# Optimization experiments

Measured on AMD Instinct MI355X. Metric: run time of the kernel, lower is better.

The kernel has to match this reference:

```python
import jax, jax.numpy as jnp
import numpy as np

NUM_HEADS = 12

def setup_inputs() -> dict:
    key = jax.random.key(0)
    ks = jax.random.split(key, 5)
    B, S, E = 1, 4096, 768
    x = jax.random.normal(ks[0], (B, S, E), dtype=jnp.float32)
    Wqkv = jax.random.normal(ks[1], (3 * E, E), dtype=jnp.float32) * (E ** -0.5)
    bqkv = jax.random.normal(ks[2], (3 * E,), dtype=jnp.float32) * 0.02
    Wo = jax.random.normal(ks[3], (E, E), dtype=jnp.float32) * (E ** -0.5)
    bo = jax.random.normal(ks[4], (E,), dtype=jnp.float32) * 0.02
    return {"x": x, "Wqkv": Wqkv, "bqkv": bqkv, "Wo": Wo, "bo": bo, "window_size": 128}

def reference(x, Wqkv, bqkv, Wo, bo, window_size):
    B, S, E = x.shape
    H = NUM_HEADS
    hd = E // H
    # qkv projection: [B,S,3E] -> [B,S,H,3*hd] -> split
    qkv = (x @ Wqkv.T + bqkv).reshape(B, S, H, 3 * hd)
    q, k, v = jnp.split(qkv, 3, axis=-1)  # each [B,S,H,hd]
    q = q.transpose(0, 2, 1, 3)  # [B,H,S,hd]
    k = k.transpose(0, 2, 1, 3)
    v = v.transpose(0, 2, 1, 3)
    # dense scores, masked to local window |i-j| <= window_size
    scores = jnp.einsum('bhqd,bhkd->bhqk', q, k) / (hd ** 0.5)
    idx = jnp.arange(S)
    in_window = jnp.abs(idx[:, None] - idx[None, :]) <= window_size  # [S,S]
    scores = jnp.where(in_window[None, None, :, :], scores, -jnp.inf)
    attn = jax.nn.softmax(scores, axis=-1)
    out = jnp.einsum('bhqk,bhkd->bhqd', attn, v)  # [B,H,S,hd]
    out = out.transpose(0, 2, 1, 3).reshape(B, S, E)
    return out @ Wo.T + bo
```

## Files before the change

kernel.cpp:

```cpp
#include <hip/hip_runtime.h>


typedef __attribute__((ext_vector_type(8))) short short8;
typedef __attribute__((ext_vector_type(4))) short short4v;
typedef __attribute__((ext_vector_type(4))) float f32x4;

#define S_LEN 4096
#define EMB   768
#define NH    12
#define HD    64
#define QT    64
#define WMAX  128
#define NKT   20
#define QSCALE 0.18033688f

#if defined(__HIP_DEVICE_COMPILE__)
#define MFMA16(a, b, c) __builtin_amdgcn_mfma_f32_16x16x16bf16_1k(a, b, c, 0, 0, 0)
#else
#define MFMA16(a, b, c) (c)
#endif

__device__ __forceinline__ short f2bf(float f) {
    union { unsigned int i; float f; } c;
    c.f = f;
    unsigned int i = c.i;
    unsigned int r = (i + 0x7FFFu + ((i >> 16) & 1u)) >> 16;
    return (short)(unsigned short)r;
}

#define NX4  (S_LEN * EMB / 4)
#define NW4  (3 * EMB * EMB / 4)
#define NO4  (EMB * EMB / 4)
__global__ __launch_bounds__(256) void convert_all(
    const float* __restrict__ x, const float* __restrict__ wqkv,
    const float* __restrict__ wo, short* __restrict__ xb,
    short* __restrict__ wqkvb, short* __restrict__ wob)
{
    int i = blockIdx.x * 256 + threadIdx.x;
    const float* src; short* dst; int off;
    if (i < NX4)            { src = x;    dst = xb;    off = i; }
    else if (i < NX4 + NW4) { src = wqkv; dst = wqkvb; off = i - NX4; }
    else                    { src = wo;   dst = wob;   off = i - NX4 - NW4; }
    float4 v = ((const float4*)src)[off];
    short4v o = { f2bf(v.x), f2bf(v.y), f2bf(v.z), f2bf(v.w) };
    *(short4v*)(dst + (size_t)off * 4) = o;
}

__global__ __launch_bounds__(256) void gemm_qkv(
    const short* __restrict__ A, const short* __restrict__ B,
    const float* __restrict__ bias, short* __restrict__ Cv,
    int M, int N, int K)
{
    __shared__ __align__(16) short smem[2 * 4096 + 2 * 3072];
    short* As0 = smem;
    short* Bs0 = smem + 2 * 4096;

    const int t = threadIdx.x;
    const int w = t >> 6, l = t & 63;
    const int quad = l >> 4, lane16 = l & 15;
    const int m0 = blockIdx.y * 128, n0 = blockIdx.x * 96;
    const int wm = (w >> 1) * 64, wn = (w & 1) * 48;

    f32x4 acc[4][3];
#pragma unroll
    for (int i = 0; i < 4; ++i)
#pragma unroll
        for (int j = 0; j < 3; ++j) acc[i][j] = (f32x4){0.f, 0.f, 0.f, 0.f};

    const int NKI = K >> 5;

    auto stage = [&](int ki, int b) {
        short* Asb = As0 + b * 4096;
        short* Bsb = Bs0 + b * 3072;
#pragma unroll
        for (int i = 0; i < 4; ++i) {
            int c = i * 256 + t;
            if (c < 512) {
                int r = c >> 2, kc = c & 3;
#if defined(__HIP_DEVICE_COMPILE__) && __has_builtin(__builtin_amdgcn_global_load_lds)
                __builtin_amdgcn_global_load_lds(
                    (const __attribute__((address_space(1))) void*)(A + (size_t)(m0 + r) * K + ki * 32 + kc * 8),
                    (__attribute__((address_space(3))) void*)(Asb + c * 8), 16, 0, 0);
#else
                *(short8*)(Asb + c * 8) = *(const short8*)(A + (size_t)(m0 + r) * K + ki * 32 + kc * 8);
#endif
            } else if (c < 896) {
                int cb = c - 512;
                int r = cb >> 2, kc = cb & 3;
#if defined(__HIP_DEVICE_COMPILE__) && __has_builtin(__builtin_amdgcn_global_load_lds)
                __builtin_amdgcn_global_load_lds(
                    (const __attribute__((address_space(1))) void*)(B + (size_t)(n0 + r) * K + ki * 32 + kc * 8),
                    (__attribute__((address_space(3))) void*)(Bsb + cb * 8), 16, 0, 0);
#else
                *(short8*)(Bsb + cb * 8) = *(const short8*)(B + (size_t)(n0 + r) * K + ki * 32 + kc * 8);
#endif
            }
        }
    };

    stage(0, 0);
    for (int kb = 0; kb < NKI; ++kb) {
        const int cur = kb & 1;
        __syncthreads();
        if (kb + 1 < NKI) stage(kb + 1, cur ^ 1);

        const short* Asb = As0 + cur * 4096;
        const short* Bsb = Bs0 + cur * 3072;
        short8 af[4], bfr[3];
#pragma unroll
        for (int mt = 0; mt < 4; ++mt)
            af[mt] = *(const short8*)(Asb + (wm + mt * 16 + lane16) * 32 + quad * 8);
#pragma unroll
        for (int nt = 0; nt < 3; ++nt)
            bfr[nt] = *(const short8*)(Bsb + (wn + nt * 16 + lane16) * 32 + quad * 8);
#pragma unroll
        for (int mt = 0; mt < 4; ++mt)
#pragma unroll
            for (int nt = 0; nt < 3; ++nt)
                acc[mt][nt] = __builtin_amdgcn_mfma_f32_16x16x32_bf16(
                    af[mt], bfr[nt], acc[mt][nt], 0, 0, 0);
    }

    __syncthreads();
    short(*Ct)[100] = (short(*)[100])smem;

#pragma unroll
    for (int nt = 0; nt < 3; ++nt) {
        int col = n0 + wn + nt * 16 + lane16;
        float bv = bias[col];
        int h = col / 192;
        int rem = col - h * 192;
        int ty = rem >> 6, d = rem & 63;
        if (ty == 2) {
            short* vt = Cv + ((size_t)2 * NH * S_LEN) * HD + ((size_t)h * HD + d) * S_LEN;
#pragma unroll
            for (int mt = 0; mt < 4; ++mt) {
                int row0 = m0 + wm + mt * 16 + quad * 4;
                short4v o = { f2bf(acc[mt][nt][0] + bv), f2bf(acc[mt][nt][1] + bv),
                              f2bf(acc[mt][nt][2] + bv), f2bf(acc[mt][nt][3] + bv) };
                *(short4v*)(vt + row0) = o;
            }
        } else {
            float s = (ty == 0) ? QSCALE : 1.f;
            int cl = wn + nt * 16 + lane16;
#pragma unroll
            for (int mt = 0; mt < 4; ++mt) {
#pragma unroll
                for (int r = 0; r < 4; ++r)
                    Ct[wm + mt * 16 + quad * 4 + r][cl] = f2bf((acc[mt][nt][r] + bv) * s);
            }
        }
    }
    __syncthreads();

#pragma unroll
    for (int pass = 0; pass < 6; ++pass) {
        int c = pass * 256 + t;
        int row = c / 12, cg = c - row * 12;
        int col0 = n0 + cg * 8;
        int h = col0 / 192;
        int rem = col0 - h * 192;
        int ty = rem >> 6;
        if (ty == 2) continue;
        int d0 = rem - ty * 64;
        short* dst = Cv + (((size_t)ty * NH + h) * S_LEN + (m0 + row)) * HD + d0;
        *(short8*)dst = *(const short8*)(&Ct[row][cg * 8]);
    }
}

__global__ __launch_bounds__(256, 3) void attn_win(
    const short* __restrict__ qsplit, const int* __restrict__ wptr,
    short* __restrict__ attn_out)
{
    __shared__ __align__(16) short KS[320 * 64];

    const int t = threadIdx.x;
    const int w = t >> 6, l = t & 63;
    const int quad = l >> 4, lane16 = l & 15;

    const int id = blockIdx.x;
    const int xcd = id & 7, j = id >> 3;
    const int h = j >> 3;
    const int q0 = ((xcd << 3) + (j & 7)) * QT;
    const int W = *wptr;
    const int kbase = q0 - WMAX;

    const short* Qh  = qsplit + (size_t)h * S_LEN * HD;
    const short* Kh  = qsplit + (size_t)(NH + h) * S_LEN * HD;
    const short* VtG = qsplit + (size_t)2 * NH * S_LEN * HD + (size_t)h * HD * S_LEN;

#pragma unroll
    for (int i = 0; i < 10; ++i) {
        int c = i * 256 + t;
        int r = c >> 3, gs = c & 7;
        int g = gs ^ (r & 7);
        int idx = min(max(kbase + r, 0), S_LEN - 1);
#if defined(__HIP_DEVICE_COMPILE__) && __has_builtin(__builtin_amdgcn_global_load_lds)
        __builtin_amdgcn_global_load_lds(
            (const __attribute__((address_space(1))) void*)(Kh + (size_t)idx * HD + g * 8),
            (__attribute__((address_space(3))) void*)(KS + c * 8), 16, 0, 0);
#else
        *(short8*)(KS + c * 8) = *(const short8*)(Kh + (size_t)idx * HD + g * 8);
#endif
    }
    const int qi = q0 + w * 16 + lane16;
    const short* qp = Qh + (size_t)qi * HD;
    short8 bq0 = *(const short8*)(qp + quad * 8);
    short8 bq1 = *(const short8*)(qp + 32 + quad * 8);

    __syncthreads();

    f32x4 sc[NKT];
    const int d7 = lane16 & 7;
    const int s0 = (quad ^ d7) * 8;
    const int s1 = ((quad + 4) ^ d7) * 8;
#pragma unroll
    for (int kt = 0; kt < NKT; ++kt) {
        const short* kp = KS + (kt * 16 + lane16) * 64;
        short8 a0 = *(const short8*)(kp + s0);
        short8 a1 = *(const short8*)(kp + s1);
        f32x4 a = (f32x4){0.f, 0.f, 0.f, 0.f};
        a = __builtin_amdgcn_mfma_f32_16x16x32_bf16(a0, bq0, a, 0, 0, 0);
        a = __builtin_amdgcn_mfma_f32_16x16x32_bf16(a1, bq1, a, 0, 0, 0);
        sc[kt] = a;
    }

    __syncthreads();

#pragma unroll
    for (int i = 0; i < 10; ++i) {
        int c = i * 256 + t;
        int d = c / 40;
        int slot = c - d * 40;
        int sg = slot >> 3, s = slot & 7;
        int g = s ^ (d & 7);
        int key0 = kbase + sg * 64 + g * 8;
        key0 = min(max(key0, 0), S_LEN - 8);
#if defined(__HIP_DEVICE_COMPILE__) && __has_builtin(__builtin_amdgcn_global_load_lds)
        __builtin_amdgcn_global_load_lds(
            (const __attribute__((address_space(1))) void*)(VtG + (size_t)d * S_LEN + key0),
            (__attribute__((address_space(3))) void*)(KS + c * 8), 16, 0, 0);
#else
        *(short8*)(KS + c * 8) = *(const short8*)(VtG + (size_t)d * S_LEN + key0);
#endif
    }

    float m = -1e30f;
#pragma unroll
    for (int kt = 0; kt < NKT; ++kt) {
#pragma unroll
        for (int r = 0; r < 4; ++r) {
            int key = kbase + kt * 16 + quad * 4 + r;
            int dd = qi - key;
            int ad = dd < 0 ? -dd : dd;
            bool valid = ((unsigned)key < S_LEN) && (ad <= W);
            float s = valid ? sc[kt][r] : -1e30f;
            sc[kt][r] = s;
            m = fmaxf(m, s);
        }
    }
    m = fmaxf(m, __shfl_xor(m, 16, 64));
    m = fmaxf(m, __shfl_xor(m, 32, 64));

    float lsum = 0.f;
#pragma unroll
    for (int kt = 0; kt < NKT; ++kt) {
#pragma unroll
        for (int r = 0; r < 4; ++r) {
            float p = exp2f(sc[kt][r] - m);
            sc[kt][r] = p;
            lsum += p;
        }
    }
    lsum += __shfl_xor(lsum, 16, 64);
    lsum += __shfl_xor(lsum, 32, 64);
    const float rl = 1.f / fmaxf(lsum, 1e-30f);

    __syncthreads();

    f32x4 oacc[4];
#pragma unroll
    for (int nt = 0; nt < 4; ++nt) oacc[nt] = (f32x4){0.f, 0.f, 0.f, 0.f};

#pragma unroll
    for (int kt = 0; kt < NKT; ++kt) {
        short4v pb = { f2bf(sc[kt][0]), f2bf(sc[kt][1]),
                       f2bf(sc[kt][2]), f2bf(sc[kt][3]) };
        int G = kt * 2 + (quad >> 1);
        int off = (G >> 3) * 64 + ((G & 7) ^ d7) * 8 + (quad & 1) * 4;
#pragma unroll
        for (int nt = 0; nt < 4; ++nt) {
            short4v va = *(const short4v*)(KS + (nt * 16 + lane16) * 320 + off);
            oacc[nt] = MFMA16(va, pb, oacc[nt]);
        }
    }

#pragma unroll
    for (int nt = 0; nt < 4; ++nt) {
        short4v ob = { f2bf(oacc[nt][0] * rl), f2bf(oacc[nt][1] * rl),
                       f2bf(oacc[nt][2] * rl), f2bf(oacc[nt][3] * rl) };
        *(short4v*)(attn_out + (size_t)qi * EMB + h * HD + nt * 16 + quad * 4) = ob;
    }
}

__global__ __launch_bounds__(256) void gemm_out64(
    const short* __restrict__ A, const short* __restrict__ B,
    const float* __restrict__ bias, float* __restrict__ C,
    int M, int N, int K)
{
    __shared__ __align__(16) short As[2][4352];
    __shared__ __align__(16) short Bs[2][4096];

    const int t = threadIdx.x;
    const int w = t >> 6, l = t & 63;
    const int quad = l >> 4, lane16 = l & 15;
    const int m0 = blockIdx.y * 64, n0 = blockIdx.x * 64;
    const int wm = (w >> 1) * 32, wn = (w & 1) * 32;

    f32x4 acc[2][2];
#pragma unroll
    for (int i = 0; i < 2; ++i)
#pragma unroll
        for (int j = 0; j < 2; ++j) acc[i][j] = (f32x4){0.f, 0.f, 0.f, 0.f};

    const int NKI = K >> 6;

    auto stage = [&](int ki, int b) {
#pragma unroll
        for (int i = 0; i < 2; ++i) {
            int c = i * 256 + t;
            int r = c >> 3, kc = c & 7;
            int g = kc ^ (r & 7);
#if defined(__HIP_DEVICE_COMPILE__) && __has_builtin(__builtin_amdgcn_global_load_lds)
            __builtin_amdgcn_global_load_lds(
                (const __attribute__((address_space(1))) void*)(A + (size_t)(m0 + r) * K + ki * 64 + g * 8),
                (__attribute__((address_space(3))) void*)(As[b] + c * 8), 16, 0, 0);
            __builtin_amdgcn_global_load_lds(
                (const __attribute__((address_space(1))) void*)(B + (size_t)(n0 + r) * K + ki * 64 + g * 8),
                (__attribute__((address_space(3))) void*)(Bs[b] + c * 8), 16, 0, 0);
#else
            *(short8*)(As[b] + c * 8) = *(const short8*)(A + (size_t)(m0 + r) * K + ki * 64 + g * 8);
            *(short8*)(Bs[b] + c * 8) = *(const short8*)(B + (size_t)(n0 + r) * K + ki * 64 + g * 8);
#endif
        }
    };

    stage(0, 0);
    for (int kb = 0; kb < NKI; ++kb) {
        const int cur = kb & 1;
        __syncthreads();
        if (kb + 1 < NKI) stage(kb + 1, cur ^ 1);

#pragma unroll
        for (int ks = 0; ks < 2; ++ks) {
            short8 af[2], bfr[2];
#pragma unroll
            for (int mt = 0; mt < 2; ++mt) {
                int row = wm + mt * 16 + lane16;
                int slot = (ks * 4 + quad) ^ (row & 7);
                af[mt] = *(const short8*)(As[cur] + row * 64 + slot * 8);
            }
#pragma unroll
            for (int nt = 0; nt < 2; ++nt) {
                int row = wn + nt * 16 + lane16;
                int slot = (ks * 4 + quad) ^ (row & 7);
                bfr[nt] = *(const short8*)(Bs[cur] + row * 64 + slot * 8);
            }
#pragma unroll
            for (int mt = 0; mt < 2; ++mt)
#pragma unroll
                for (int nt = 0; nt < 2; ++nt)
                    acc[mt][nt] = __builtin_amdgcn_mfma_f32_16x16x32_bf16(
                        af[mt], bfr[nt], acc[mt][nt], 0, 0, 0);
        }
    }

    __syncthreads();
    float(*Ct)[66] = (float(*)[66])As;

#pragma unroll
    for (int nt = 0; nt < 2; ++nt) {
        int cl = wn + nt * 16 + lane16;
        float bv = bias[n0 + cl];
#pragma unroll
        for (int mt = 0; mt < 2; ++mt) {
#pragma unroll
            for (int r = 0; r < 4; ++r)
                Ct[wm + mt * 16 + quad * 4 + r][cl] = acc[mt][nt][r] + bv;
        }
    }
    __syncthreads();

#pragma unroll
    for (int pass = 0; pass < 4; ++pass) {
        int c = pass * 256 + t;
        int row = c >> 4, cg = c & 15;
        float4 v = { Ct[row][cg * 4], Ct[row][cg * 4 + 1],
                     Ct[row][cg * 4 + 2], Ct[row][cg * 4 + 3] };
        *(float4*)(C + (size_t)(m0 + row) * N + n0 + cg * 4) = v;
    }
}

extern "C" void kernel_launch(void* const* d_in, const int* in_sizes, int n_in,
                              void* d_out, int out_size, void* d_ws, size_t ws_size,
                              hipStream_t stream) {
    const float* x    = (const float*)d_in[0];
    const float* Wqkv = (const float*)d_in[1];
    const float* bqkv = (const float*)d_in[2];
    const float* Wo   = (const float*)d_in[3];
    const float* bo   = (const float*)d_in[4];
    const int*   wptr = (const int*)d_in[5];

    float* out = (float*)d_out;

    short* xb     = (short*)d_ws;
    short* wqkvb  = xb     + (size_t)S_LEN * EMB;
    short* wob    = wqkvb  + (size_t)3 * EMB * EMB;
    short* qsplit = wob    + (size_t)EMB * EMB;
    short* attn   = qsplit + (size_t)3 * NH * S_LEN * HD;

    dim3 blk(256);
    convert_all<<<dim3((NX4 + NW4 + NO4) / 256), blk, 0, stream>>>(
        x, Wqkv, Wo, xb, wqkvb, wob);
    gemm_qkv<<<dim3(2304 / 96, S_LEN / 128), blk, 0, stream>>>(
        xb, wqkvb, bqkv, qsplit, S_LEN, 2304, EMB);
    attn_win<<<dim3(S_LEN / QT * NH), blk, 0, stream>>>(qsplit, wptr, attn);
    gemm_out64<<<dim3(EMB / 64, S_LEN / 64), blk, 0, stream>>>(
        attn, wob, bo, out, S_LEN, EMB, EMB);
}
```

Before: 134.2 us.

## Fuse fp32-to-bf16 conversion into GEMM tile loads and drop convert kernel

Removes the separate conversion kernel that turned x, Wqkv and Wo into bf16 copies in workspace. Both GEMMs now load fp32 tiles into registers, convert them to bf16 and write them to LDS after the MFMA work of the current stage, giving a register-staged software pipeline. This saves one launch and a full read/write pass over the inputs. In exchange the GEMMs read twice the bytes per tile (fp32), re-convert weights in every block that uses them, and lose the async global-to-LDS load path.

```diff
diff --git a/kernel.cpp b/kernel.cpp
--- a/kernel.cpp
+++ b/kernel.cpp
@@ -27,27 +27,15 @@
     unsigned int r = (i + 0x7FFFu + ((i >> 16) & 1u)) >> 16;
     return (short)(unsigned short)r;
 }
-
-#define NX4  (S_LEN * EMB / 4)
-#define NW4  (3 * EMB * EMB / 4)
-#define NO4  (EMB * EMB / 4)
-__global__ __launch_bounds__(256) void convert_all(
-    const float* __restrict__ x, const float* __restrict__ wqkv,
-    const float* __restrict__ wo, short* __restrict__ xb,
-    short* __restrict__ wqkvb, short* __restrict__ wob)
-{
-    int i = blockIdx.x * 256 + threadIdx.x;
-    const float* src; short* dst; int off;
-    if (i < NX4)            { src = x;    dst = xb;    off = i; }
-    else if (i < NX4 + NW4) { src = wqkv; dst = wqkvb; off = i - NX4; }
-    else                    { src = wo;   dst = wob;   off = i - NX4 - NW4; }
-    float4 v = ((const float4*)src)[off];
-    short4v o = { f2bf(v.x), f2bf(v.y), f2bf(v.z), f2bf(v.w) };
-    *(short4v*)(dst + (size_t)off * 4) = o;
+__device__ __forceinline__ short8 cvt8(f32x4 a, f32x4 b) {
+    short8 o;
+#pragma unroll
+    for (int j = 0; j < 4; ++j) { o[j] = f2bf(a[j]); o[4 + j] = f2bf(b[j]); }
+    return o;
 }
 
 __global__ __launch_bounds__(256) void gemm_qkv(
-    const short* __restrict__ A, const short* __restrict__ B,
+    const float* __restrict__ A, const float* __restrict__ B,
     const float* __restrict__ bias, short* __restrict__ Cv,
     int M, int N, int K)
 {
@@ -69,40 +57,50 @@
 
     const int NKI = K >> 5;
 
-    auto stage = [&](int ki, int b) {
+    f32x4 ra[2][2], rb[2][2];
+
+    auto loadg = [&](int ki) {
+#pragma unroll
+        for (int i = 0; i < 2; ++i) {
+            int c = i * 256 + t;
+            int r = c >> 2, kc = c & 3;
+            const float* p = A + (size_t)(m0 + r) * K + ki * 32 + kc * 8;
+            ra[i][0] = *(const f32x4*)p;
+            ra[i][1] = *(const f32x4*)(p + 4);
+        }
+        {
+            int r = t >> 2, kc = t & 3;
+            const float* p = B + (size_t)(n0 + r) * K + ki * 32 + kc * 8;
+            rb[0][0] = *(const f32x4*)p;
+            rb[0][1] = *(const f32x4*)(p + 4);
+        }
+        if (t < 128) {
+            int cb = 256 + t;
+            int r = cb >> 2, kc = cb & 3;
+            const float* p = B + (size_t)(n0 + r) * K + ki * 32 + kc * 8;
+            rb[1][0] = *(const f32x4*)p;
+            rb[1][1] = *(const f32x4*)(p + 4);
+        }
+    };
+    auto cvtwrite = [&](int b) {
         short* Asb = As0 + b * 4096;
         short* Bsb = Bs0 + b * 3072;
 #pragma unroll
-        for (int i = 0; i < 4; ++i) {
+        for (int i = 0; i < 2; ++i) {
             int c = i * 256 + t;
-            if (c < 512) {
-                int r = c >> 2, kc = c & 3;
-#if defined(__HIP_DEVICE_COMPILE__) && __has_builtin(__builtin_amdgcn_global_load_lds)
-                __builtin_amdgcn_global_load_lds(
-                    (const __attribute__((address_space(1))) void*)(A + (size_t)(m0 + r) * K + ki * 32 + kc * 8),
-                    (__attribute__((address_space(3))) void*)(Asb + c * 8), 16, 0, 0);
-#else
-                *(short8*)(Asb + c * 8) = *(const short8*)(A + (size_t)(m0 + r) * K + ki * 32 + kc * 8);
-#endif
-            } else if (c < 896) {
-                int cb = c - 512;
-                int r = cb >> 2, kc = cb & 3;
-#if defined(__HIP_DEVICE_COMPILE__) && __has_builtin(__builtin_amdgcn_global_load_lds)
-                __builtin_amdgcn_global_load_lds(
-                    (const __attribute__((address_space(1))) void*)(B + (size_t)(n0 + r) * K + ki * 32 + kc * 8),
-                    (__attribute__((address_space(3))) void*)(Bsb + cb * 8), 16, 0, 0);
-#else
-                *(short8*)(Bsb + cb * 8) = *(const short8*)(B + (size_t)(n0 + r) * K + ki * 32 + kc * 8);
-#endif
-            }
-        }
+            *(short8*)(Asb + c * 8) = cvt8(ra[i][0], ra[i][1]);
+        }
+        *(short8*)(Bsb + t * 8) = cvt8(rb[0][0], rb[0][1]);
+        if (t < 128)
+            *(short8*)(Bsb + (256 + t) * 8) = cvt8(rb[1][0], rb[1][1]);
     };
 
-    stage(0, 0);
+    loadg(0);
+    cvtwrite(0);
     for (int kb = 0; kb < NKI; ++kb) {
         const int cur = kb & 1;
         __syncthreads();
-        if (kb + 1 < NKI) stage(kb + 1, cur ^ 1);
+        if (kb + 1 < NKI) loadg(kb + 1);
 
         const short* Asb = As0 + cur * 4096;
         const short* Bsb = Bs0 + cur * 3072;
@@ -119,6 +117,8 @@
             for (int nt = 0; nt < 3; ++nt)
                 acc[mt][nt] = __builtin_amdgcn_mfma_f32_16x16x32_bf16(
                     af[mt], bfr[nt], acc[mt][nt], 0, 0, 0);
+
+        if (kb + 1 < NKI) cvtwrite(cur ^ 1);
     }
 
     __syncthreads();
@@ -304,7 +304,7 @@
 }
 
 __global__ __launch_bounds__(256) void gemm_out64(
-    const short* __restrict__ A, const short* __restrict__ B,
+    const short* __restrict__ A, const float* __restrict__ Bf,
     const float* __restrict__ bias, float* __restrict__ C,
     int M, int N, int K)
 {
@@ -325,7 +325,7 @@
 
     const int NKI = K >> 6;
 
-    auto stage = [&](int ki, int b) {
+    auto stageA = [&](int ki, int b) {
 #pragma unroll
         for (int i = 0; i < 2; ++i) {
             int c = i * 256 + t;
@@ -335,21 +335,40 @@
             __builtin_amdgcn_global_load_lds(
                 (const __attribute__((address_space(1))) void*)(A + (size_t)(m0 + r) * K + ki * 64 + g * 8),
                 (__attribute__((address_space(3))) void*)(As[b] + c * 8), 16, 0, 0);
-            __builtin_amdgcn_global_load_lds(
-                (const __attribute__((address_space(1))) void*)(B + (size_t)(n0 + r) * K + ki * 64 + g * 8),
-                (__attribute__((address_space(3))) void*)(Bs[b] + c * 8), 16, 0, 0);
 #else
             *(short8*)(As[b] + c * 8) = *(const short8*)(A + (size_t)(m0 + r) * K + ki * 64 + g * 8);
-            *(short8*)(Bs[b] + c * 8) = *(const short8*)(B + (size_t)(n0 + r) * K + ki * 64 + g * 8);
 #endif
         }
     };
 
-    stage(0, 0);
+    f32x4 rbB[2][2];
+    auto loadB = [&](int ki) {
+#pragma unroll
+        for (int i = 0; i < 2; ++i) {
+            int c = i * 256 + t;
+            int r = c >> 3, gs = c & 7;
+            const float* p = Bf + (size_t)(n0 + r) * K + ki * 64 + gs * 8;
+            rbB[i][0] = *(const f32x4*)p;
+            rbB[i][1] = *(const f32x4*)(p + 4);
+        }
+    };
+    auto writeB = [&](int b) {
+#pragma unroll
+        for (int i = 0; i < 2; ++i) {
+            int c = i * 256 + t;
+            int r = c >> 3, gs = c & 7;
+            int slot = gs ^ (r & 7);
+            *(short8*)(Bs[b] + (r * 8 + slot) * 8) = cvt8(rbB[i][0], rbB[i][1]);
+        }
+    };
+
+    stageA(0, 0);
+    loadB(0);
+    writeB(0);
     for (int kb = 0; kb < NKI; ++kb) {
         const int cur = kb & 1;
         __syncthreads();
-        if (kb + 1 < NKI) stage(kb + 1, cur ^ 1);
+        if (kb + 1 < NKI) { stageA(kb + 1, cur ^ 1); loadB(kb + 1); }
 
 #pragma unroll
         for (int ks = 0; ks < 2; ++ks) {
@@ -373,6 +392,8 @@
                     acc[mt][nt] = __builtin_amdgcn_mfma_f32_16x16x32_bf16(
                         af[mt], bfr[nt], acc[mt][nt], 0, 0, 0);
         }
+
+        if (kb + 1 < NKI) writeB(cur ^ 1);
     }
 
     __syncthreads();
@@ -413,18 +434,13 @@
 
     float* out = (float*)d_out;
 
-    short* xb     = (short*)d_ws;
-    short* wqkvb  = xb     + (size_t)S_LEN * EMB;
-    short* wob    = wqkvb  + (size_t)3 * EMB * EMB;
-    short* qsplit = wob    + (size_t)EMB * EMB;
+    short* qsplit = (short*)d_ws;
     short* attn   = qsplit + (size_t)3 * NH * S_LEN * HD;
 
     dim3 blk(256);
-    convert_all<<<dim3((NX4 + NW4 + NO4) / 256), blk, 0, stream>>>(
-        x, Wqkv, Wo, xb, wqkvb, wob);
     gemm_qkv<<<dim3(2304 / 96, S_LEN / 128), blk, 0, stream>>>(
-        xb, wqkvb, bqkv, qsplit, S_LEN, 2304, EMB);
+        x, Wqkv, bqkv, qsplit, S_LEN, 2304, EMB);
     attn_win<<<dim3(S_LEN / QT * NH), blk, 0, stream>>>(qsplit, wptr, attn);
     gemm_out64<<<dim3(EMB / 64, S_LEN / 64), blk, 0, stream>>>(
-        attn, wob, bo, out, S_LEN, EMB, EMB);
-}
+        attn, Wo, bo, out, S_LEN, EMB, EMB);
+}
```

Result: slower. 139.8 us (+4.1%).
